# Performance work log

Hardware: AMD Instinct MI355X
Metric: run time of the kernel (lower is better)

The kernel has to match this reference:

```python
import jax, jax.numpy as jnp
import numpy as np

B, S, H, I, E = 4, 4096, 1024, 4096, 4
VOCAB = 32000


def setup_inputs() -> dict:
    key = jax.random.key(0)
    k1, k2, k3, k4, k5 = jax.random.split(key, 5)
    scale = 1.0 / np.sqrt(H)
    return {
        "hidden_states": jax.random.normal(k1, (B, S, H), dtype=jnp.float32),
        "gate_proj": jax.random.normal(k2, (E, H, I), dtype=jnp.float32) * scale,
        "up_proj": jax.random.normal(k3, (E, H, I), dtype=jnp.float32) * scale,
        "down_proj": jax.random.normal(k4, (E, I, H), dtype=jnp.float32) * (1.0 / np.sqrt(I)),
        "token_ids": jax.random.randint(k5, (B, S), 0, VOCAB, dtype=jnp.int64),
    }


def reference(hidden_states, gate_proj, up_proj, down_proj, token_ids):
    # hidden_states: [B, S, H]; token_ids: [B, S]
    num_experts = gate_proj.shape[0]
    expert_ids = token_ids % num_experts  # [B, S]
    out = jnp.zeros_like(hidden_states)
    for e in range(num_experts):  # small fixed expert loop
        gate = jax.nn.silu(jnp.einsum("bsh,hi->bsi", hidden_states, gate_proj[e]))
        up = jnp.einsum("bsh,hi->bsi", hidden_states, up_proj[e])
        y = jnp.einsum("bsi,ih->bsh", gate * up, down_proj[e])
        out = jnp.where((expert_ids == e)[..., None], y, out)
    return out
```

## Files before the change

### kernel.cpp

```cpp
#include <hip/hip_runtime.h>

#define TOK    16384
#define HD     1024
#define ID     4096
#define NE     4
#define MAXMT  131

typedef __attribute__((ext_vector_type(4))) float f32x4;
typedef __attribute__((ext_vector_type(8))) short bf16x8;
typedef unsigned int u32;

static __device__ __forceinline__ unsigned short f2bf(float f) {
  unsigned u = __float_as_uint(f);
  u += 0x7FFFu + ((u >> 16) & 1u);
  return (unsigned short)(u >> 16);
}

static __device__ __forceinline__ void gl16(const void* g, void* l) {
  __builtin_amdgcn_global_load_lds((const __attribute__((address_space(1))) u32*)g,
                                   (__attribute__((address_space(3))) u32*)l, 16, 0, 0);
}

static __device__ __forceinline__ void barx() {
  asm volatile("" ::: "memory");
  __builtin_amdgcn_s_barrier();
  asm volatile("" ::: "memory");
}

__global__ void k_route0(const int* __restrict__ ids, int* __restrict__ meta) {
  __shared__ int cnt[4];
  int t = threadIdx.x;
  if (t < 4) cnt[t] = 0;
  __syncthreads();
  int l0 = 0, l1 = 0, l2 = 0, l3 = 0;
  for (int i = t; i < TOK; i += 256) {
    int e = ids[i] & 3;
    l0 += (e == 0); l1 += (e == 1); l2 += (e == 2); l3 += (e == 3);
  }
  atomicAdd(&cnt[0], l0); atomicAdd(&cnt[1], l1);
  atomicAdd(&cnt[2], l2); atomicAdd(&cnt[3], l3);
  __syncthreads();
  if (t == 0) {
    int o = 0;
    for (int e = 0; e < 4; ++e) { meta[e] = o; meta[8 + e] = o; o += cnt[e]; }
    meta[4] = o;
  }
}

__global__ void k_route1(const int* __restrict__ ids, int* __restrict__ meta,
                         int* __restrict__ perm) {
  int i = blockIdx.x * 256 + threadIdx.x;
  if (i < TOK) {
    int e = ids[i] & 3;
    int s = atomicAdd(&meta[8 + e], 1);
    perm[s] = i;
  }
}

__global__ void k_conv(const float* __restrict__ s, unsigned short* __restrict__ d, int n8) {
  int i = blockIdx.x * blockDim.x + threadIdx.x;
  int st = gridDim.x * blockDim.x;
  for (; i < n8; i += st) {
    const f32x4* p = (const f32x4*)(s + ((size_t)i << 3));
    f32x4 a = p[0], b = p[1];
    union { unsigned short u[8]; uint4 q; } o;
    o.u[0] = f2bf(a.x); o.u[1] = f2bf(a.y); o.u[2] = f2bf(a.z); o.u[3] = f2bf(a.w);
    o.u[4] = f2bf(b.x); o.u[5] = f2bf(b.y); o.u[6] = f2bf(b.z); o.u[7] = f2bf(b.w);
    *(uint4*)(d + ((size_t)i << 3)) = o.q;
  }
}

__global__ void k_tr12(const float* __restrict__ gw, const float* __restrict__ uw,
                       const float* __restrict__ dw, unsigned short* __restrict__ gT,
                       unsigned short* __restrict__ uT, unsigned short* __restrict__ dT) {
  __shared__ float tile[64][65];
  int z = blockIdx.y;
  const float* s; unsigned short* d; int R, C, lg;
  if (z < 8) {
    R = HD; C = ID; lg = 6;
    int m = z & 3;
    if (z < 4) { s = gw + (size_t)m * R * C; d = gT + (size_t)m * R * C; }
    else       { s = uw + (size_t)m * R * C; d = uT + (size_t)m * R * C; }
  } else {
    R = ID; C = HD; lg = 4;
    int m = z - 8;
    s = dw + (size_t)m * R * C; d = dT + (size_t)m * R * C;
  }
  int bx = blockIdx.x;
  int tx = bx & ((1 << lg) - 1), ty = bx >> lg;
  int r0 = ty << 6, c0 = tx << 6;
  int t = threadIdx.x;
  int lr = t >> 4, lc = (t & 15) << 2;
  #pragma unroll
  for (int it = 0; it < 4; ++it) {
    int r = lr + (it << 4);
    f32x4 v = *(const f32x4*)(s + (size_t)(r0 + r) * C + c0 + lc);
    tile[r][lc] = v.x; tile[r][lc + 1] = v.y; tile[r][lc + 2] = v.z; tile[r][lc + 3] = v.w;
  }
  __syncthreads();
  int c = t >> 2, rb = (t & 3) << 4;
  union { unsigned short u[16]; uint4 q[2]; } o;
  #pragma unroll
  for (int j = 0; j < 16; ++j) o.u[j] = f2bf(tile[rb + j][c]);
  uint4* dp = (uint4*)(d + (size_t)(c0 + c) * R + r0 + rb);
  dp[0] = o.q[0]; dp[1] = o.q[1];
}

#define MFMA16 __builtin_amdgcn_mfma_f32_16x16x32_bf16

__global__ __launch_bounds__(256, 2) void k_gemm1(
    const unsigned short* __restrict__ hid,
    const unsigned short* __restrict__ gT,
    const unsigned short* __restrict__ uT,
    const int* __restrict__ meta,
    const int* __restrict__ perm,
    unsigned short* __restrict__ act) {
  __shared__ __align__(16) char smem[49152];
  int offs[5];
  #pragma unroll
  for (int i = 0; i < 5; ++i) offs[i] = meta[i];
  int bid = blockIdx.x;
  int logical = (bid & 7) * (MAXMT * 32 / 8) + (bid >> 3);
  int mt = logical >> 5;
  int ny = logical & 31;
  int e = -1, mloc = 0, base = 0;
  #pragma unroll
  for (int ee = 0; ee < 4; ++ee) {
    int tiles = (offs[ee + 1] - offs[ee] + 127) >> 7;
    if (e < 0 && mt < base + tiles) { e = ee; mloc = mt - base; }
    base += tiles;
  }
  if (e < 0) return;
  int slot0 = offs[e] + (mloc << 7);
  int send = offs[e + 1];
  int tid = threadIdx.x, lane = tid & 63, wid = tid >> 6;
  int n0 = ny << 7;

  const unsigned short* gb = gT + (size_t)e * ID * HD;
  const unsigned short* ub = uT + (size_t)e * ID * HD;
  int rsub = tid >> 3;
  int ks = tid & 7;
  const unsigned short* srcA[4];
  const unsigned short* srcG[4];
  const unsigned short* srcU[4];
  #pragma unroll
  for (int j = 0; j < 4; ++j) {
    int r = j * 32 + rsub;
    int ko = (ks ^ (r & 7)) << 3;
    int slot = slot0 + r;
    int pr = perm[slot < send ? slot : slot0];
    srcA[j] = hid + (size_t)pr * HD + ko;
    srcG[j] = gb + (size_t)(n0 + r) * HD + ko;
    srcU[j] = ub + (size_t)(n0 + r) * HD + ko;
  }
  int dstl = tid << 4;

  int wm = wid >> 1, wn = wid & 1;
  int r16 = lane & 15, kg = lane >> 4;
  int offA[4], offG[4], offU[4];
  #pragma unroll
  for (int m = 0; m < 4; ++m) {
    int r = wm * 64 + m * 16 + r16;
    offA[m] = r * 128 + ((kg ^ (r & 7)) << 4);
  }
  #pragma unroll
  for (int n = 0; n < 4; ++n) {
    int r = wn * 64 + n * 16 + r16;
    int o = r * 128 + ((kg ^ (r & 7)) << 4);
    offG[n] = 16384 + o;
    offU[n] = 32768 + o;
  }

  f32x4 ag[4][4], au[4][4];
  #pragma unroll
  for (int m = 0; m < 4; ++m)
    #pragma unroll
    for (int n = 0; n < 4; ++n) { ag[m][n] = (f32x4){0,0,0,0}; au[m][n] = (f32x4){0,0,0,0}; }

  for (int t = 0; t < HD / 64; ++t) {
    barx();
    int ko = t * 64;
    #pragma unroll
    for (int j = 0; j < 4; ++j) gl16(srcA[j] + ko, smem + j * 4096 + dstl);
    #pragma unroll
    for (int j = 0; j < 4; ++j) gl16(srcG[j] + ko, smem + 16384 + j * 4096 + dstl);
    #pragma unroll
    for (int j = 0; j < 4; ++j) gl16(srcU[j] + ko, smem + 32768 + j * 4096 + dstl);
    asm volatile("s_waitcnt vmcnt(0)" ::: "memory");
    barx();
    #pragma unroll
    for (int kk = 0; kk < 2; ++kk) {
      bf16x8 fa[4], fg[4], fu[4];
      #pragma unroll
      for (int m = 0; m < 4; ++m) fa[m] = *(const bf16x8*)(smem + (offA[m] ^ (kk << 6)));
      #pragma unroll
      for (int n = 0; n < 4; ++n) {
        fg[n] = *(const bf16x8*)(smem + (offG[n] ^ (kk << 6)));
        fu[n] = *(const bf16x8*)(smem + (offU[n] ^ (kk << 6)));
      }
      #pragma unroll
      for (int m = 0; m < 4; ++m)
        #pragma unroll
        for (int n = 0; n < 4; ++n) {
          ag[m][n] = MFMA16(fa[m], fg[n], ag[m][n], 0, 0, 0);
          au[m][n] = MFMA16(fa[m], fu[n], au[m][n], 0, 0, 0);
        }
    }
  }

  #pragma unroll
  for (int m = 0; m < 4; ++m) {
    int lr = (wm << 6) + (m << 4) + (kg << 2);
    #pragma unroll
    for (int n = 0; n < 4; ++n) {
      int col = n0 + (wn << 6) + (n << 4) + r16;
      #pragma unroll
      for (int r = 0; r < 4; ++r) {
        int slot = slot0 + lr + r;
        if (slot < send) {
          float g = ag[m][n][r];
          float u = au[m][n][r];
          float y = (g / (1.f + __expf(-g))) * u;
          act[(size_t)slot * ID + col] = f2bf(y);
        }
      }
    }
  }
}

__global__ __launch_bounds__(256, 3) void k_gemm2(
    const unsigned short* __restrict__ act,
    const unsigned short* __restrict__ dT,
    const int* __restrict__ meta,
    const int* __restrict__ perm,
    float* __restrict__ out) {
  __shared__ __align__(16) char smem[32768];
  int offs[5];
  #pragma unroll
  for (int i = 0; i < 5; ++i) offs[i] = meta[i];
  int bid = blockIdx.x;
  int logical = (bid & 7) * (MAXMT * 8 / 8) + (bid >> 3);
  int mt = logical >> 3;
  int nyy = logical & 7;
  int e = -1, mloc = 0, base = 0;
  #pragma unroll
  for (int ee = 0; ee < 4; ++ee) {
    int tiles = (offs[ee + 1] - offs[ee] + 127) >> 7;
    if (e < 0 && mt < base + tiles) { e = ee; mloc = mt - base; }
    base += tiles;
  }
  if (e < 0) return;
  int slot0 = offs[e] + (mloc << 7);
  int send = offs[e + 1];
  int tid = threadIdx.x, lane = tid & 63, wid = tid >> 6;
  int n0 = nyy << 7;
  const unsigned short* dbase = dT + (size_t)e * HD * ID;

  int rsub = tid >> 3;
  int ks = tid & 7;
  const unsigned short* srcA[4];
  const unsigned short* srcB[4];
  #pragma unroll
  for (int j = 0; j < 4; ++j) {
    int r = j * 32 + rsub;
    int ko = (ks ^ (r & 7)) << 3;
    int slot = slot0 + r;
    int s2 = slot < send ? slot : slot0;
    srcA[j] = act + (size_t)s2 * ID + ko;
    srcB[j] = dbase + (size_t)(n0 + r) * ID + ko;
  }
  int dstl = tid << 4;

  int wm = wid >> 1, wn = wid & 1;
  int r16 = lane & 15, kg = lane >> 4;
  int offA[4], offB[4];
  #pragma unroll
  for (int m = 0; m < 4; ++m) {
    int r = wm * 64 + m * 16 + r16;
    offA[m] = r * 128 + ((kg ^ (r & 7)) << 4);
  }
  #pragma unroll
  for (int n = 0; n < 4; ++n) {
    int r = wn * 64 + n * 16 + r16;
    offB[n] = 16384 + r * 128 + ((kg ^ (r & 7)) << 4);
  }

  f32x4 acc[4][4];
  #pragma unroll
  for (int m = 0; m < 4; ++m)
    #pragma unroll
    for (int n = 0; n < 4; ++n) acc[m][n] = (f32x4){0,0,0,0};

  for (int t = 0; t < ID / 64; ++t) {
    barx();
    int ko = t * 64;
    #pragma unroll
    for (int j = 0; j < 4; ++j) gl16(srcA[j] + ko, smem + j * 4096 + dstl);
    #pragma unroll
    for (int j = 0; j < 4; ++j) gl16(srcB[j] + ko, smem + 16384 + j * 4096 + dstl);
    asm volatile("s_waitcnt vmcnt(0)" ::: "memory");
    barx();
    #pragma unroll
    for (int kk = 0; kk < 2; ++kk) {
      bf16x8 fa[4], fb[4];
      #pragma unroll
      for (int m = 0; m < 4; ++m) fa[m] = *(const bf16x8*)(smem + (offA[m] ^ (kk << 6)));
      #pragma unroll
      for (int n = 0; n < 4; ++n) fb[n] = *(const bf16x8*)(smem + (offB[n] ^ (kk << 6)));
      #pragma unroll
      for (int m = 0; m < 4; ++m)
        #pragma unroll
        for (int n = 0; n < 4; ++n)
          acc[m][n] = MFMA16(fa[m], fb[n], acc[m][n], 0, 0, 0);
    }
  }

  #pragma unroll
  for (int m = 0; m < 4; ++m) {
    int lr = (wm << 6) + (m << 4) + (kg << 2);
    int pr4[4];
    #pragma unroll
    for (int r = 0; r < 4; ++r) {
      int slot = slot0 + lr + r;
      pr4[r] = slot < send ? perm[slot] : -1;
    }
    #pragma unroll
    for (int n = 0; n < 4; ++n) {
      int col = n0 + (wn << 6) + (n << 4) + r16;
      #pragma unroll
      for (int r = 0; r < 4; ++r) {
        if (pr4[r] >= 0) out[(size_t)pr4[r] * HD + col] = acc[m][n][r];
      }
    }
  }
}

extern "C" void kernel_launch(void* const* d_in, const int* in_sizes, int n_in,
                              void* d_out, int out_size, void* d_ws, size_t ws_size,
                              hipStream_t stream) {
  const float* hs = (const float*)d_in[0];
  const float* gw = (const float*)d_in[1];
  const float* uw = (const float*)d_in[2];
  const float* dw = (const float*)d_in[3];
  const int* ids = (const int*)d_in[4];
  float* out = (float*)d_out;

  char* w = (char*)d_ws;
  size_t o = 0;
  int* meta = (int*)(w + o); o += 64;
  int* perm = (int*)(w + o); o += (size_t)TOK * 4;
  o = (o + 255) & ~(size_t)255;
  unsigned short* hid = (unsigned short*)(w + o); o += (size_t)TOK * HD * 2;
  unsigned short* gT  = (unsigned short*)(w + o); o += (size_t)NE * ID * HD * 2;
  unsigned short* uT  = (unsigned short*)(w + o); o += (size_t)NE * ID * HD * 2;
  unsigned short* dT  = (unsigned short*)(w + o); o += (size_t)NE * ID * HD * 2;
  unsigned short* actb = (unsigned short*)(w + o); o += (size_t)TOK * ID * 2;

  hipLaunchKernelGGL(k_route0, dim3(1), dim3(256), 0, stream, ids, meta);
  hipLaunchKernelGGL(k_route1, dim3(TOK / 256), dim3(256), 0, stream, ids, meta, perm);
  hipLaunchKernelGGL(k_conv, dim3(2048), dim3(256), 0, stream, hs, hid, TOK * HD / 8);
  hipLaunchKernelGGL(k_tr12, dim3(1024, 12), dim3(256), 0, stream, gw, uw, dw, gT, uT, dT);
  hipLaunchKernelGGL(k_gemm1, dim3(MAXMT * 32), dim3(256), 0, stream,
                     hid, gT, uT, meta, perm, actb);
  hipLaunchKernelGGL(k_gemm2, dim3(MAXMT * 8), dim3(256), 0, stream,
                     actb, dT, meta, perm, out);
}
```

Measured before the change: 714.2 us.

## Load A operand fragments directly from global memory into registers, bypassing LDS

Both grouped GEMM kernels now read the token-side A operand (hidden states and activations) straight from global memory into MFMA fragment registers. Only the weight tiles still go through LDS, which shrinks shared memory per block and removes the LDS write and read traffic for A. The trade is that A rows are no longer shared across the two column-warps, so each row is fetched twice from global or L2. The per-lane 16-byte loads on gathered rows may also coalesce poorly, and these global loads sit behind the same vmcnt wait as the LDS loads.

After: 997.3 us. 1.4x slower.

```diff
diff --git a/kernel.cpp b/kernel.cpp
--- a/kernel.cpp
+++ b/kernel.cpp
@@ -115,7 +115,7 @@
     const int* __restrict__ meta,
     const int* __restrict__ perm,
     unsigned short* __restrict__ act) {
-  __shared__ __align__(16) char smem[49152];
+  __shared__ __align__(16) char smem[32768];
   int offs[5];
   #pragma unroll
   for (int i = 0; i < 5; ++i) offs[i] = meta[i];
@@ -140,16 +140,12 @@
   const unsigned short* ub = uT + (size_t)e * ID * HD;
   int rsub = tid >> 3;
   int ks = tid & 7;
-  const unsigned short* srcA[4];
   const unsigned short* srcG[4];
   const unsigned short* srcU[4];
   #pragma unroll
   for (int j = 0; j < 4; ++j) {
     int r = j * 32 + rsub;
     int ko = (ks ^ (r & 7)) << 3;
-    int slot = slot0 + r;
-    int pr = perm[slot < send ? slot : slot0];
-    srcA[j] = hid + (size_t)pr * HD + ko;
     srcG[j] = gb + (size_t)(n0 + r) * HD + ko;
     srcU[j] = ub + (size_t)(n0 + r) * HD + ko;
   }
@@ -157,18 +153,22 @@
 
   int wm = wid >> 1, wn = wid & 1;
   int r16 = lane & 15, kg = lane >> 4;
-  int offA[4], offG[4], offU[4];
+  u32 offAg[4];
   #pragma unroll
   for (int m = 0; m < 4; ++m) {
-    int r = wm * 64 + m * 16 + r16;
-    offA[m] = r * 128 + ((kg ^ (r & 7)) << 4);
-  }
+    int row = wm * 64 + m * 16 + r16;
+    int slot = slot0 + row;
+    int pr = perm[slot < send ? slot : slot0];
+    offAg[m] = (u32)pr * HD + (u32)(kg * 8);
+  }
+
+  int offG[4], offU[4];
   #pragma unroll
   for (int n = 0; n < 4; ++n) {
     int r = wn * 64 + n * 16 + r16;
     int o = r * 128 + ((kg ^ (r & 7)) << 4);
-    offG[n] = 16384 + o;
-    offU[n] = 32768 + o;
+    offG[n] = o;
+    offU[n] = 16384 + o;
   }
 
   f32x4 ag[4][4], au[4][4];
@@ -181,30 +181,34 @@
     barx();
     int ko = t * 64;
     #pragma unroll
-    for (int j = 0; j < 4; ++j) gl16(srcA[j] + ko, smem + j * 4096 + dstl);
-    #pragma unroll
-    for (int j = 0; j < 4; ++j) gl16(srcG[j] + ko, smem + 16384 + j * 4096 + dstl);
-    #pragma unroll
-    for (int j = 0; j < 4; ++j) gl16(srcU[j] + ko, smem + 32768 + j * 4096 + dstl);
+    for (int j = 0; j < 4; ++j) gl16(srcG[j] + ko, smem + j * 4096 + dstl);
+    #pragma unroll
+    for (int j = 0; j < 4; ++j) gl16(srcU[j] + ko, smem + 16384 + j * 4096 + dstl);
+    bf16x8 fa0[4], fa1[4];
+    #pragma unroll
+    for (int m = 0; m < 4; ++m) {
+      fa0[m] = *(const bf16x8*)(hid + offAg[m] + ko);
+      fa1[m] = *(const bf16x8*)(hid + offAg[m] + ko + 32);
+    }
     asm volatile("s_waitcnt vmcnt(0)" ::: "memory");
     barx();
     #pragma unroll
     for (int kk = 0; kk < 2; ++kk) {
-      bf16x8 fa[4], fg[4], fu[4];
-      #pragma unroll
-      for (int m = 0; m < 4; ++m) fa[m] = *(const bf16x8*)(smem + (offA[m] ^ (kk << 6)));
+      bf16x8 fg[4], fu[4];
       #pragma unroll
       for (int n = 0; n < 4; ++n) {
         fg[n] = *(const bf16x8*)(smem + (offG[n] ^ (kk << 6)));
         fu[n] = *(const bf16x8*)(smem + (offU[n] ^ (kk << 6)));
       }
       #pragma unroll
-      for (int m = 0; m < 4; ++m)
+      for (int m = 0; m < 4; ++m) {
+        bf16x8 fa = kk ? fa1[m] : fa0[m];
         #pragma unroll
         for (int n = 0; n < 4; ++n) {
-          ag[m][n] = MFMA16(fa[m], fg[n], ag[m][n], 0, 0, 0);
-          au[m][n] = MFMA16(fa[m], fu[n], au[m][n], 0, 0, 0);
+          ag[m][n] = MFMA16(fa, fg[n], ag[m][n], 0, 0, 0);
+          au[m][n] = MFMA16(fa, fu[n], au[m][n], 0, 0, 0);
         }
+      }
     }
   }
 
@@ -234,7 +238,7 @@
     const int* __restrict__ meta,
     const int* __restrict__ perm,
     float* __restrict__ out) {
-  __shared__ __align__(16) char smem[32768];
+  __shared__ __align__(16) char smem[16384];
   int offs[5];
   #pragma unroll
   for (int i = 0; i < 5; ++i) offs[i] = meta[i];
@@ -258,31 +262,30 @@
 
   int rsub = tid >> 3;
   int ks = tid & 7;
-  const unsigned short* srcA[4];
   const unsigned short* srcB[4];
   #pragma unroll
   for (int j = 0; j < 4; ++j) {
     int r = j * 32 + rsub;
     int ko = (ks ^ (r & 7)) << 3;
-    int slot = slot0 + r;
-    int s2 = slot < send ? slot : slot0;
-    srcA[j] = act + (size_t)s2 * ID + ko;
     srcB[j] = dbase + (size_t)(n0 + r) * ID + ko;
   }
   int dstl = tid << 4;
 
   int wm = wid >> 1, wn = wid & 1;
   int r16 = lane & 15, kg = lane >> 4;
-  int offA[4], offB[4];
+  u32 offAg[4];
   #pragma unroll
   for (int m = 0; m < 4; ++m) {
-    int r = wm * 64 + m * 16 + r16;
-    offA[m] = r * 128 + ((kg ^ (r & 7)) << 4);
-  }
+    int row = wm * 64 + m * 16 + r16;
+    int slot = slot0 + row;
+    int s2 = slot < send ? slot : slot0;
+    offAg[m] = (u32)s2 * ID + (u32)(kg * 8);
+  }
+  int offB[4];
   #pragma unroll
   for (int n = 0; n < 4; ++n) {
     int r = wn * 64 + n * 16 + r16;
-    offB[n] = 16384 + r * 128 + ((kg ^ (r & 7)) << 4);
+    offB[n] = r * 128 + ((kg ^ (r & 7)) << 4);
   }
 
   f32x4 acc[4][4];
@@ -295,23 +298,27 @@
     barx();
     int ko = t * 64;
     #pragma unroll
-    for (int j = 0; j < 4; ++j) gl16(srcA[j] + ko, smem + j * 4096 + dstl);
-    #pragma unroll
-    for (int j = 0; j < 4; ++j) gl16(srcB[j] + ko, smem + 16384 + j * 4096 + dstl);
+    for (int j = 0; j < 4; ++j) gl16(srcB[j] + ko, smem + j * 4096 + dstl);
+    bf16x8 fa0[4], fa1[4];
+    #pragma unroll
+    for (int m = 0; m < 4; ++m) {
+      fa0[m] = *(const bf16x8*)(act + offAg[m] + ko);
+      fa1[m] = *(const bf16x8*)(act + offAg[m] + ko + 32);
+    }
     asm volatile("s_waitcnt vmcnt(0)" ::: "memory");
     barx();
     #pragma unroll
     for (int kk = 0; kk < 2; ++kk) {
-      bf16x8 fa[4], fb[4];
-      #pragma unroll
-      for (int m = 0; m < 4; ++m) fa[m] = *(const bf16x8*)(smem + (offA[m] ^ (kk << 6)));
+      bf16x8 fb[4];
       #pragma unroll
       for (int n = 0; n < 4; ++n) fb[n] = *(const bf16x8*)(smem + (offB[n] ^ (kk << 6)));
       #pragma unroll
-      for (int m = 0; m < 4; ++m)
+      for (int m = 0; m < 4; ++m) {
+        bf16x8 fa = kk ? fa1[m] : fa0[m];
         #pragma unroll
         for (int n = 0; n < 4; ++n)
-          acc[m][n] = MFMA16(fa[m], fb[n], acc[m][n], 0, 0, 0);
+          acc[m][n] = MFMA16(fa, fb[n], acc[m][n], 0, 0, 0);
+      }
     }
   }
 
```
